# Performance work log

Measured on AMD Instinct MI355X. Metric: run time of the kernel, lower is better.

The kernel has to match this reference:

```python
import math
import jax, jax.numpy as jnp
import numpy as np

MAX_LEN = 1024

def _sinusoidal_pe(seq_len, d_model):
    pos = jnp.arange(seq_len, dtype=jnp.float32)[:, None]
    div = jnp.exp(jnp.arange(0, d_model, 2, dtype=jnp.float32) * (-math.log(10000.0) / d_model))
    ang = pos * div  # [S, D/2]
    pe = jnp.zeros((seq_len, d_model), dtype=jnp.float32)
    pe = pe.at[:, 0::2].set(jnp.sin(ang))
    pe = pe.at[:, 1::2].set(jnp.cos(ang))
    return pe

def setup_inputs() -> dict:
    key = jax.random.key(0)
    ks = jax.random.split(key, 4)
    B, S, D, H = 4, 1024, 1024, 16
    x = jax.random.normal(ks[0], (B, S, D), dtype=jnp.float32)
    gamma = jnp.ones((D,), dtype=jnp.float32)
    beta = jnp.zeros((D,), dtype=jnp.float32)
    w_pos = jax.random.normal(ks[1], (2 * D, D), dtype=jnp.float32) * (1.0 / math.sqrt(D))
    w_tok = jax.random.normal(ks[2], (3 * D, D), dtype=jnp.float32) * (1.0 / math.sqrt(D))
    bias_table = jax.random.normal(ks[3], (2 * MAX_LEN, H), dtype=jnp.float32) * 0.02
    return {"x": x, "gamma": gamma, "beta": beta, "w_pos": w_pos, "w_tok": w_tok, "bias_table": bias_table}

def reference(x, gamma, beta, w_pos, w_tok, bias_table):
    B, S, D = x.shape
    H = bias_table.shape[1]
    dh = D // H
    scale = 1.0 / math.sqrt(2 * dh)

    # untied positional scores (identical across batch)
    pe = _sinusoidal_pe(S, D)                      # [S, D]
    pos = pe @ w_pos.T                             # [S, 2D]
    pos_k, pos_q = pos[:, :D], pos[:, D:]
    pos_k = pos_k.reshape(S, H, dh)
    pos_q = pos_q.reshape(S, H, dh)
    pos_attn = jnp.einsum('qhd,khd->hqk', pos_q, pos_k)  # [H, S, S]

    # token scores
    mu = jnp.mean(x, axis=-1, keepdims=True)
    var = jnp.mean((x - mu) ** 2, axis=-1, keepdims=True)
    xn = (x - mu) / jnp.sqrt(var + 1e-5) * gamma + beta
    tok = xn @ w_tok.T                             # [B, S, 3D]
    tok_k, tok_q, tok_v = jnp.split(tok, 3, axis=-1)
    tok_k = tok_k.reshape(B, S, H, dh)
    tok_q = tok_q.reshape(B, S, H, dh)
    tok_v = tok_v.reshape(B, S, H, dh)
    tok_attn = jnp.einsum('bqhd,bkhd->bhqk', tok_q, tok_k)  # [B, H, S, S]

    attn = (tok_attn + pos_attn[None]) / scale

    # relative-position bias
    rel = jnp.arange(S)[None, :] - jnp.arange(S)[:, None] + MAX_LEN  # [S, S]
    bias = bias_table[rel]                         # [S, S, H]
    attn = attn + jnp.transpose(bias, (2, 0, 1))[None]

    attn = jax.nn.softmax(attn, axis=-1)
    out = jnp.einsum('bhqk,bkhd->bqhd', attn, tok_v)
    return out.reshape(B, S, D)
```

## Files before the change

kernel.cpp:

```cpp
#include <hip/hip_runtime.h>
#include <math.h>

#define SB 1024
#define DM 1024
#define BB 4
#define NH 16
#define DH 64
#define ML 1024

typedef __attribute__((ext_vector_type(8))) short short8;
typedef __attribute__((ext_vector_type(8))) _Float16 half8;
typedef __attribute__((ext_vector_type(4))) float f32x4;
typedef unsigned short u16;

#define S_BARRIER() __builtin_amdgcn_s_barrier()
#define SCHED_FENCE() __builtin_amdgcn_sched_barrier(0)
#define WAITV(N) asm volatile("s_waitcnt vmcnt(" #N ")" ::: "memory")
#define WAITLGKM() asm volatile("s_waitcnt lgkmcnt(0)" ::: "memory")
#define WAITVL() asm volatile("s_waitcnt vmcnt(0) lgkmcnt(0)" ::: "memory")

__device__ __forceinline__ u16 f2bf(float x) {
  unsigned u = __float_as_uint(x);
  u += 0x7fffu + ((u >> 16) & 1u);
  return (u16)(u >> 16);
}
__device__ __forceinline__ float bf2f(u16 h) { return __uint_as_float((unsigned)h << 16); }

__device__ __forceinline__ void async16(void* lds, const void* g) {
  __builtin_amdgcn_global_load_lds(
      (const __attribute__((address_space(1))) unsigned*)g,
      (__attribute__((address_space(3))) unsigned*)lds, 16, 0, 0);
}


__device__ __forceinline__ void pack16_body(int rt, int t, const float* __restrict__ src,
    _Float16* __restrict__ dH, _Float16* __restrict__ dL, float scale) {
  int r16 = t >> 4, ks = t & 15;
  const float* sp = src + (size_t)(rt * 16 + r16) * 1024 + ks * 64;
  float v[64];
  #pragma unroll
  for (int i = 0; i < 16; ++i) {
    float4 f = *(const float4*)(sp + i * 4);
    v[i*4+0] = f.x; v[i*4+1] = f.y; v[i*4+2] = f.z; v[i*4+3] = f.w;
  }
  #pragma unroll
  for (int hf = 0; hf < 2; ++hf) {
    int kt = ks * 2 + hf;
    #pragma unroll
    for (int gg = 0; gg < 4; ++gg) {
      half8 hv, lv;
      #pragma unroll
      for (int j = 0; j < 8; ++j) {
        float x = v[hf * 32 + gg * 8 + j] * scale;
        _Float16 h = (_Float16)x;
        hv[j] = h;
        lv[j] = (_Float16)(x - (float)h);
      }
      size_t off = ((size_t)(rt * 32 + kt) * 64 + r16 + gg * 16) * 8;
      *(half8*)(dH + off) = hv;
      *(half8*)(dL + off) = lv;
    }
  }
}

__device__ __forceinline__ void pe_pack_body(int rt, int t,
    _Float16* __restrict__ dH, _Float16* __restrict__ dL) {
  int r16 = t >> 4, ks = t & 15;
  int p = rt * 16 + r16;
  float v[64];
  #pragma unroll
  for (int i = 0; i < 32; ++i) {
    int c0 = ks * 64 + 2 * i;
    float div = expf((float)c0 * (-9.210340371976184f / (float)DM));
    float ang = (float)p * div;
    v[2*i]   = sinf(ang);
    v[2*i+1] = cosf(ang);
  }
  #pragma unroll
  for (int hf = 0; hf < 2; ++hf) {
    int kt = ks * 2 + hf;
    #pragma unroll
    for (int gg = 0; gg < 4; ++gg) {
      half8 hv, lv;
      #pragma unroll
      for (int j = 0; j < 8; ++j) {
        float x = v[hf * 32 + gg * 8 + j];
        _Float16 h = (_Float16)x;
        hv[j] = h;
        lv[j] = (_Float16)(x - (float)h);
      }
      size_t off = ((size_t)(rt * 32 + kt) * 64 + r16 + gg * 16) * 8;
      *(half8*)(dH + off) = hv;
      *(half8*)(dL + off) = lv;
    }
  }
}

__device__ __forceinline__ void ln_pack_body(int rt, int t, const float* __restrict__ x,
    const float* __restrict__ gamma, const float* __restrict__ beta,
    _Float16* __restrict__ dH, _Float16* __restrict__ dL) {
  int r16 = t >> 4, ks = t & 15;
  const float* sp = x + (size_t)(rt * 16 + r16) * 1024 + ks * 64;
  float v[64];
  float s1 = 0.f, s2 = 0.f;
  #pragma unroll
  for (int i = 0; i < 16; ++i) {
    float4 f = *(const float4*)(sp + i * 4);
    v[i*4+0] = f.x; v[i*4+1] = f.y; v[i*4+2] = f.z; v[i*4+3] = f.w;
    s1 += f.x + f.y + f.z + f.w;
    s2 += f.x*f.x + f.y*f.y + f.z*f.z + f.w*f.w;
  }
  #pragma unroll
  for (int off = 1; off < 16; off <<= 1) {
    s1 += __shfl_xor(s1, off, 64);
    s2 += __shfl_xor(s2, off, 64);
  }
  float mu = s1 * (1.0f / 1024.0f);
  float var = s2 * (1.0f / 1024.0f) - mu * mu;
  float rstd = rsqrtf(var + 1e-5f);
  #pragma unroll
  for (int hf = 0; hf < 2; ++hf) {
    int kt = ks * 2 + hf;
    #pragma unroll
    for (int gg = 0; gg < 4; ++gg) {
      const float* gp = gamma + ks * 64 + hf * 32 + gg * 8;
      const float* bp = beta  + ks * 64 + hf * 32 + gg * 8;
      half8 hv, lv;
      #pragma unroll
      for (int j = 0; j < 8; ++j) {
        float xn = (v[hf * 32 + gg * 8 + j] - mu) * rstd * gp[j] + bp[j];
        _Float16 h = (_Float16)xn;
        hv[j] = h;
        lv[j] = (_Float16)(xn - (float)h);
      }
      size_t off = ((size_t)(rt * 32 + kt) * 64 + r16 + gg * 16) * 8;
      *(half8*)(dH + off) = hv;
      *(half8*)(dL + off) = lv;
    }
  }
}

__global__ __launch_bounds__(256) void prep_all(
    const float* __restrict__ x, const float* __restrict__ gamma,
    const float* __restrict__ beta,
    const float* __restrict__ w_pos, const float* __restrict__ w_tok,
    _Float16* __restrict__ peH, _Float16* __restrict__ peL,
    _Float16* __restrict__ xnH, _Float16* __restrict__ xnL,
    _Float16* __restrict__ wpH, _Float16* __restrict__ wpL,
    _Float16* __restrict__ wtH, _Float16* __restrict__ wtL) {
  int bid = blockIdx.x;
  int t = threadIdx.x;
  if (bid < 64)       pe_pack_body(bid, t, peH, peL);
  else if (bid < 320) ln_pack_body(bid - 64, t, x, gamma, beta, xnH, xnL);
  else if (bid < 448) pack16_body(bid - 320, t, w_pos, wpH, wpL, 32.0f);
  else                pack16_body(bid - 448, t, w_tok, wtH, wtL, 32.0f);
}


__device__ __forceinline__ void stage_gemm(bool split, int wv, int lane,
    _Float16* Lb, const _Float16* AH, const _Float16* AL, const _Float16* BH,
    int mt0, int nt0, int kt) {
  if (split) {
    #pragma unroll
    for (int rd = 0; rd < 8; ++rd) {
      int ci = rd * 4 + wv;
      const _Float16* src;
      if (ci < 16) {
        int mt = ci >> 1, pl = ci & 1;
        src = (pl ? AL : AH) + ((size_t)((mt0 + mt) * 32 + kt) * 64 + lane) * 8;
      } else {
        src = BH + ((size_t)((nt0 + ci - 16) * 32 + kt) * 64 + lane) * 8;
      }
      async16(&Lb[ci * 512], src);
    }
  } else {
    #pragma unroll
    for (int rd = 0; rd < 6; ++rd) {
      int idx = wv * 6 + rd;
      int ci = (idx < 8) ? (idx * 2) : (idx + 8);
      const _Float16* src;
      if (ci < 16) {
        src = AH + ((size_t)((mt0 + (ci >> 1)) * 32 + kt) * 64 + lane) * 8;
      } else {
        src = BH + ((size_t)((nt0 + ci - 16) * 32 + kt) * 64 + lane) * 8;
      }
      async16(&Lb[ci * 512], src);
    }
  }
}

__global__ __launch_bounds__(256, 2) void gemm16p(
    const _Float16* __restrict__ AtH, const _Float16* __restrict__ AtL,
    const _Float16* __restrict__ ApH, const _Float16* __restrict__ ApL,
    const _Float16* __restrict__ BtH, const _Float16* __restrict__ BtL,
    const _Float16* __restrict__ BpH, const _Float16* __restrict__ BpL,
    u16* __restrict__ KtfH, u16* __restrict__ KtfL,
    u16* __restrict__ KpfH, u16* __restrict__ KpfL,
    u16* __restrict__ QH, u16* __restrict__ QL,
    u16* __restrict__ pQH, u16* __restrict__ pQL,
    u16* __restrict__ vF, float sK, float sQ, float sV) {
  __shared__ _Float16 L[2][32 * 512];
  int t = threadIdx.x;
  int wv = t >> 6, lane = t & 63;
  int wm = wv >> 1, wn = wv & 1;
  int r16 = lane & 15, g = lane >> 4;

  int phys = blockIdx.x;
  int bid = (phys & 7) * 56 + (phys >> 3);
  bool isPos = (bid >= 384);
  int idx = isPos ? bid - 384 : bid;
  int n0, m0;
  const _Float16 *AH, *AL, *BH, *BL;
  if (isPos) { n0 = (idx & 7) * 256;  m0 = (idx >> 3) * 128;
               AH = ApH; AL = ApL; BH = BpH; BL = BpL; }
  else       { n0 = (idx % 12) * 256; m0 = (idx / 12) * 128;
               AH = AtH; AL = AtL; BH = BtH; BL = BtL; }
  int mt0 = m0 >> 4, nt0 = n0 >> 4;
  bool split = isPos || (n0 < 2048);

  f32x4 acc[4][8];
  #pragma unroll
  for (int i = 0; i < 4; ++i)
    #pragma unroll
    for (int j = 0; j < 8; ++j) acc[i][j] = (f32x4){0.f, 0.f, 0.f, 0.f};

  stage_gemm(split, wv, lane, &L[0][0], AH, AL, BH, mt0, nt0, 0);

  for (int kt = 0; kt < 32; ++kt) {
    _Float16* Lc = &L[kt & 1][0];
    half8 blo[8];
    if (split) {
      #pragma unroll
      for (int j = 0; j < 8; ++j) {
        int ntg = nt0 + wn * 8 + j;
        blo[j] = *(const half8*)(BL + ((size_t)(ntg * 32 + kt) * 64 + lane) * 8);
      }
    }
    SCHED_FENCE();
    if (kt < 31)
      stage_gemm(split, wv, lane, &L[(kt + 1) & 1][0], AH, AL, BH, mt0, nt0, kt + 1);
    if (split) { if (kt < 31) WAITV(16); else WAITV(8); }
    else       { if (kt < 31) WAITV(6);  else WAITV(0); }
    S_BARRIER();
    SCHED_FENCE();

    half8 ah[4], al[4];
    #pragma unroll
    for (int i = 0; i < 4; ++i)
      ah[i] = *(const half8*)&Lc[(((wm * 4 + i) * 2 + 0) * 512) + lane * 8];
    if (split) {
      #pragma unroll
      for (int i = 0; i < 4; ++i)
        al[i] = *(const half8*)&Lc[(((wm * 4 + i) * 2 + 1) * 512) + lane * 8];
    }
    #pragma unroll
    for (int j = 0; j < 8; ++j) {
      half8 bh = *(const half8*)&Lc[((16 + wn * 8 + j) * 512) + lane * 8];
      #pragma unroll
      for (int i = 0; i < 4; ++i) {
        acc[i][j] = __builtin_amdgcn_mfma_f32_16x16x32_f16(ah[i], bh, acc[i][j], 0, 0, 0);
        if (split) {
          acc[i][j] = __builtin_amdgcn_mfma_f32_16x16x32_f16(al[i], bh, acc[i][j], 0, 0, 0);
          acc[i][j] = __builtin_amdgcn_mfma_f32_16x16x32_f16(ah[i], blo[j], acc[i][j], 0, 0, 0);
        }
      }
    }
    WAITLGKM();
    S_BARRIER();
    SCHED_FENCE();
  }

  int band = n0 >> 10;
  u16* fKH = isPos ? KpfH : KtfH;
  u16* fKL = isPos ? KpfL : KtfL;
  u16* qHo = isPos ? pQH  : QH;
  u16* qLo = isPos ? pQL  : QL;
  if (band == 1) {
    #pragma unroll
    for (int i = 0; i < 4; ++i)
      #pragma unroll
      for (int j = 0; j < 8; ++j) {
        int lc = (n0 & 1023) + wn * 128 + j * 16 + r16;
        #pragma unroll
        for (int reg = 0; reg < 4; ++reg) {
          int row = m0 + wm * 64 + i * 16 + g * 4 + reg;
          float cv = acc[i][j][reg] * sQ;
          u16 hi = f2bf(cv);
          qHo[(size_t)row * 1024 + lc] = hi;
          qLo[(size_t)row * 1024 + lc] = f2bf(cv - bf2f(hi));
        }
      }
  } else if (band == 0) {
    #pragma unroll
    for (int i = 0; i < 4; ++i)
      #pragma unroll
      for (int j = 0; j < 8; ++j) {
        int colg = n0 + wn * 128 + j * 16 + r16;
        int h = colg >> 6, dc = colg & 63;
        #pragma unroll
        for (int reg = 0; reg < 4; ++reg) {
          int row = m0 + wm * 64 + i * 16 + g * 4 + reg;
          int bhK = (row >> 10) * NH + h;
          size_t a = ((size_t)((bhK * 64 + ((row & 1023) >> 4)) * 2 + (dc >> 5)) << 9)
                   + ((row & 15) + 16 * ((dc >> 3) & 3)) * 8 + (dc & 7);
          float cv = acc[i][j][reg] * sK;
          u16 hi = f2bf(cv);
          fKH[a] = hi;
          fKL[a] = f2bf(cv - bf2f(hi));
        }
      }
  } else {
    #pragma unroll
    for (int i = 0; i < 4; ++i)
      #pragma unroll
      for (int j = 0; j < 8; ++j) {
        int colg = (n0 & 1023) + wn * 128 + j * 16 + r16;
        int h = colg >> 6, dc = colg & 63;
        #pragma unroll
        for (int reg = 0; reg < 4; ++reg) {
          int row = m0 + wm * 64 + i * 16 + g * 4 + reg;
          int s = row & 1023;
          size_t a = ((size_t)((((row >> 10) * NH + h) * 32 + (s >> 5)) * 4 + (dc >> 4)) << 9)
                   + ((s >> 3) & 3) * 128 + (s & 7) + (dc & 15) * 8;
          vF[a] = f2bf(acc[i][j][reg] * sV);
        }
      }
  }
}

__global__ __launch_bounds__(256, 2) void gemm16m(
    const _Float16* __restrict__ AtH, const _Float16* __restrict__ AtL,
    const _Float16* __restrict__ ApH, const _Float16* __restrict__ ApL,
    const float* __restrict__ Wt, const float* __restrict__ Wp,
    u16* __restrict__ KtfH, u16* __restrict__ KtfL,
    u16* __restrict__ KpfH, u16* __restrict__ KpfL,
    u16* __restrict__ QH, u16* __restrict__ QL,
    u16* __restrict__ pQH, u16* __restrict__ pQL,
    u16* __restrict__ vF, float sK, float sQ, float sV) {
  __shared__ _Float16 L[48 * 512];
  int t = threadIdx.x;
  int wv = t >> 6, lane = t & 63;
  int wm = wv >> 1, wn = wv & 1;
  int r16 = lane & 15, g = lane >> 4;

  int phys = blockIdx.x;
  int bid = (phys & 7) * 56 + (phys >> 3);
  bool isPos = (bid >= 384);
  int idx = isPos ? bid - 384 : bid;
  int n0, m0;
  const _Float16 *AH, *AL;
  const float* W;
  if (isPos) { n0 = (idx & 7) * 256;  m0 = (idx >> 3) * 128; AH = ApH; AL = ApL; W = Wp; }
  else       { n0 = (idx % 12) * 256; m0 = (idx / 12) * 128; AH = AtH; AL = AtL; W = Wt; }
  int mt0 = m0 >> 4, nt0 = n0 >> 4;
  bool split = isPos || (n0 < 2048);

  f32x4 acc[4][8];
  #pragma unroll
  for (int i = 0; i < 4; ++i)
    #pragma unroll
    for (int j = 0; j < 8; ++j) acc[i][j] = (f32x4){0.f, 0.f, 0.f, 0.f};

  for (int kt = 0; kt < 32; ++kt) {
    __syncthreads();
    #pragma unroll
    for (int rd = 0; rd < 4; ++rd) {
      int ci = rd * 4 + wv;
      int mt = ci >> 1, pl = ci & 1;
      if (!split && pl) continue;
      const _Float16* src = (pl ? AL : AH)
          + ((size_t)((mt0 + mt) * 32 + kt) * 64 + lane) * 8;
      async16(&L[ci * 512], src);
    }
    #pragma unroll
    for (int tt = 0; tt < 4; ++tt) {
      int nt = wv * 4 + tt;
      const float* wsrc = W + (size_t)((nt0 + nt) * 16 + r16) * 1024 + kt * 32 + g * 8;
      float4 w0 = *(const float4*)wsrc;
      float4 w1 = *(const float4*)(wsrc + 4);
      float wvv[8] = {w0.x, w0.y, w0.z, w0.w, w1.x, w1.y, w1.z, w1.w};
      half8 hv, lv;
      #pragma unroll
      for (int j = 0; j < 8; ++j) {
        float xx = wvv[j] * 32.0f;
        _Float16 h = (_Float16)xx;
        hv[j] = h;
        lv[j] = (_Float16)(xx - (float)h);
      }
      *(half8*)&L[(16 + nt) * 512 + lane * 8] = hv;
      if (split) *(half8*)&L[(32 + nt) * 512 + lane * 8] = lv;
    }
    __syncthreads();

    half8 ah[4], al[4];
    #pragma unroll
    for (int i = 0; i < 4; ++i)
      ah[i] = *(const half8*)&L[(((wm * 4 + i) * 2 + 0) * 512) + lane * 8];
    if (split) {
      #pragma unroll
      for (int i = 0; i < 4; ++i)
        al[i] = *(const half8*)&L[(((wm * 4 + i) * 2 + 1) * 512) + lane * 8];
    }
    #pragma unroll
    for (int j = 0; j < 8; ++j) {
      half8 bh = *(const half8*)&L[((16 + wn * 8 + j) * 512) + lane * 8];
      #pragma unroll
      for (int i = 0; i < 4; ++i) {
        acc[i][j] = __builtin_amdgcn_mfma_f32_16x16x32_f16(ah[i], bh, acc[i][j], 0, 0, 0);
        if (split) {
          half8 bl = *(const half8*)&L[((32 + wn * 8 + j) * 512) + lane * 8];
          acc[i][j] = __builtin_amdgcn_mfma_f32_16x16x32_f16(al[i], bh, acc[i][j], 0, 0, 0);
          acc[i][j] = __builtin_amdgcn_mfma_f32_16x16x32_f16(ah[i], bl, acc[i][j], 0, 0, 0);
        }
      }
    }
  }

  int band = n0 >> 10;
  u16* fKH = isPos ? KpfH : KtfH;
  u16* fKL = isPos ? KpfL : KtfL;
  u16* qHo = isPos ? pQH  : QH;
  u16* qLo = isPos ? pQL  : QL;
  if (band == 1) {
    #pragma unroll
    for (int i = 0; i < 4; ++i)
      #pragma unroll
      for (int j = 0; j < 8; ++j) {
        int lc = (n0 & 1023) + wn * 128 + j * 16 + r16;
        #pragma unroll
        for (int reg = 0; reg < 4; ++reg) {
          int row = m0 + wm * 64 + i * 16 + g * 4 + reg;
          float cv = acc[i][j][reg] * sQ;
          u16 hi = f2bf(cv);
          qHo[(size_t)row * 1024 + lc] = hi;
          qLo[(size_t)row * 1024 + lc] = f2bf(cv - bf2f(hi));
        }
      }
  } else if (band == 0) {
    #pragma unroll
    for (int i = 0; i < 4; ++i)
      #pragma unroll
      for (int j = 0; j < 8; ++j) {
        int colg = n0 + wn * 128 + j * 16 + r16;
        int h = colg >> 6, dc = colg & 63;
        #pragma unroll
        for (int reg = 0; reg < 4; ++reg) {
          int row = m0 + wm * 64 + i * 16 + g * 4 + reg;
          int bhK = (row >> 10) * NH + h;
          size_t a = ((size_t)((bhK * 64 + ((row & 1023) >> 4)) * 2 + (dc >> 5)) << 9)
                   + ((row & 15) + 16 * ((dc >> 3) & 3)) * 8 + (dc & 7);
          float cv = acc[i][j][reg] * sK;
          u16 hi = f2bf(cv);
          fKH[a] = hi;
          fKL[a] = f2bf(cv - bf2f(hi));
        }
      }
  } else {
    #pragma unroll
    for (int i = 0; i < 4; ++i)
      #pragma unroll
      for (int j = 0; j < 8; ++j) {
        int colg = (n0 & 1023) + wn * 128 + j * 16 + r16;
        int h = colg >> 6, dc = colg & 63;
        #pragma unroll
        for (int reg = 0; reg < 4; ++reg) {
          int row = m0 + wm * 64 + i * 16 + g * 4 + reg;
          int s = row & 1023;
          size_t a = ((size_t)((((row >> 10) * NH + h) * 32 + (s >> 5)) * 4 + (dc >> 4)) << 9)
                   + ((s >> 3) & 3) * 128 + (s & 7) + (dc & 15) * 8;
          vF[a] = f2bf(acc[i][j][reg] * sV);
        }
      }
  }
}

__device__ __forceinline__ void stage_attn(u16* Klds,
    const u16* ktH, const u16* ktL, const u16* kpH, const u16* kpL,
    const u16* vb, int wv, int lo) {
  int p0 = wv * 512, p1 = (wv + 4) * 512;
  async16(&Klds[0 * 4096 + p0], ktH + p0 + lo);
  async16(&Klds[0 * 4096 + p1], ktH + p1 + lo);
  async16(&Klds[1 * 4096 + p0], ktL + p0 + lo);
  async16(&Klds[1 * 4096 + p1], ktL + p1 + lo);
  async16(&Klds[2 * 4096 + p0], kpH + p0 + lo);
  async16(&Klds[2 * 4096 + p1], kpH + p1 + lo);
  async16(&Klds[3 * 4096 + p0], kpL + p0 + lo);
  async16(&Klds[3 * 4096 + p1], kpL + p1 + lo);
  async16(&Klds[4 * 4096 + p0], vb + p0 + lo);
  async16(&Klds[4 * 4096 + p1], vb + p1 + lo);
}

__global__ __launch_bounds__(256, 2) void attn_mfma11(
    const u16* __restrict__ KtfH, const u16* __restrict__ KtfL,
    const u16* __restrict__ KpfH, const u16* __restrict__ KpfL,
    const u16* __restrict__ QHg, const u16* __restrict__ QLg,
    const u16* __restrict__ pQH, const u16* __restrict__ pQL,
    const u16* __restrict__ Vf,
    const float* __restrict__ bt,
    float* __restrict__ out) {
  __shared__ u16 Klds[5 * 4096];
  __shared__ float biasL[2 * ML];
  __shared__ u16 Pb[4][16 * 72];

  int phys = blockIdx.x;
  int bid = (phys & 7) * 64 + (phys >> 3);
  int qt = bid & 7;
  int bh = bid >> 3;
  int b = bh >> 4, h = bh & 15;
  int q0 = qt * 128;
  int t = threadIdx.x;
  int wv = t >> 6, lane = t & 63;
  int g = lane >> 4, r16 = lane & 15;
  int lo = lane * 8;

  #pragma unroll
  for (int k = 0; k < 8; ++k)
    biasL[t + k * 256] = bt[(size_t)(t + k * 256) * NH + h];

  short8 qhi[2][4], qlo[2][4];
  #pragma unroll
  for (int cc = 0; cc < 2; ++cc) {
    int qrow = q0 + wv * 32 + cc * 16 + r16;
    #pragma unroll
    for (int c = 0; c < 4; ++c) {
      if (c < 2) {
        size_t off = (size_t)(b * SB + qrow) * 1024 + h * DH + c * 32 + g * 8;
        qhi[cc][c] = *(const short8*)(QHg + off);
        qlo[cc][c] = *(const short8*)(QLg + off);
      } else {
        size_t off = (size_t)qrow * 1024 + h * DH + (c - 2) * 32 + g * 8;
        qhi[cc][c] = *(const short8*)(pQH + off);
        qlo[cc][c] = *(const short8*)(pQL + off);
      }
    }
  }

  f32x4 O[2][4];
  #pragma unroll
  for (int cc = 0; cc < 2; ++cc)
    #pragma unroll
    for (int dt = 0; dt < 4; ++dt) O[cc][dt] = (f32x4){0.f, 0.f, 0.f, 0.f};
  float m_run[2][4], l_run[2][4];
  #pragma unroll
  for (int cc = 0; cc < 2; ++cc)
    #pragma unroll
    for (int reg = 0; reg < 4; ++reg) { m_run[cc][reg] = -3e38f; l_run[cc][reg] = 0.f; }

  int qb0 = q0 + wv * 32 + g * 4;
  const u16* ktHb = KtfH + (size_t)(bh * 64) * 1024;
  const u16* ktLb = KtfL + (size_t)(bh * 64) * 1024;
  const u16* kpHb = KpfH + (size_t)(h * 64) * 1024;
  const u16* kpLb = KpfL + (size_t)(h * 64) * 1024;
  const u16* vb   = Vf   + (size_t)(bh * 32) * 2048;
  int bb = ML + r16 - qb0;

  stage_attn(Klds, ktHb, ktLb, kpHb, kpLb, vb, wv, lo);

  for (int ktr = 0; ktr < 16; ++ktr) {
    WAITVL();
    S_BARRIER();
    SCHED_FENCE();

    float bias[2][4][4];
    #pragma unroll
    for (int nt = 0; nt < 4; ++nt)
      #pragma unroll
      for (int reg = 0; reg < 4; ++reg) {
        bias[0][nt][reg] = biasL[bb + nt * 16 - reg];
        bias[1][nt][reg] = biasL[bb - 16 + nt * 16 - reg];
      }

    f32x4 S[2][4];
    #pragma unroll
    for (int nt = 0; nt < 4; ++nt) {
      f32x4 a0 = (f32x4){0.f, 0.f, 0.f, 0.f};
      f32x4 a1 = (f32x4){0.f, 0.f, 0.f, 0.f};
      #pragma unroll
      for (int c = 0; c < 4; ++c) {
        int ch = (c < 2) ? 0 : 2;
        int co = c & 1;
        short8 bhi = *(const short8*)&Klds[(ch + 0) * 4096 + nt * 1024 + co * 512 + lo];
        short8 blo = *(const short8*)&Klds[(ch + 1) * 4096 + nt * 1024 + co * 512 + lo];
        a0 = __builtin_amdgcn_mfma_f32_16x16x32_bf16(qhi[0][c], bhi, a0, 0, 0, 0);
        a1 = __builtin_amdgcn_mfma_f32_16x16x32_bf16(qhi[1][c], bhi, a1, 0, 0, 0);
        a0 = __builtin_amdgcn_mfma_f32_16x16x32_bf16(qlo[0][c], bhi, a0, 0, 0, 0);
        a1 = __builtin_amdgcn_mfma_f32_16x16x32_bf16(qlo[1][c], bhi, a1, 0, 0, 0);
        a0 = __builtin_amdgcn_mfma_f32_16x16x32_bf16(qhi[0][c], blo, a0, 0, 0, 0);
        a1 = __builtin_amdgcn_mfma_f32_16x16x32_bf16(qhi[1][c], blo, a1, 0, 0, 0);
      }
      S[0][nt] = a0; S[1][nt] = a1;
    }

    short8 vfrag[2][4];
    #pragma unroll
    for (int kc = 0; kc < 2; ++kc)
      #pragma unroll
      for (int dt = 0; dt < 4; ++dt)
        vfrag[kc][dt] = *(const short8*)&Klds[4 * 4096 + (kc * 4 + dt) * 512 + lo];

    WAITLGKM();
    S_BARRIER();
    SCHED_FENCE();
    if (ktr < 15) {
      ktHb += 4096; ktLb += 4096; kpHb += 4096; kpLb += 4096; vb += 4096;
      stage_attn(Klds, ktHb, ktLb, kpHb, kpLb, vb, wv, lo);
    }
    SCHED_FENCE();

    #pragma unroll
    for (int cc = 0; cc < 2; ++cc)
      #pragma unroll
      for (int nt = 0; nt < 4; ++nt)
        #pragma unroll
        for (int reg = 0; reg < 4; ++reg)
          S[cc][nt][reg] += bias[cc][nt][reg];

    float tm[2][4], al[2][4];
    #pragma unroll
    for (int cc = 0; cc < 2; ++cc)
      #pragma unroll
      for (int reg = 0; reg < 4; ++reg)
        tm[cc][reg] = fmaxf(fmaxf(S[cc][0][reg], S[cc][1][reg]),
                            fmaxf(S[cc][2][reg], S[cc][3][reg]));
    #pragma unroll
    for (int off = 1; off < 16; off <<= 1)
      #pragma unroll
      for (int cc = 0; cc < 2; ++cc)
        #pragma unroll
        for (int reg = 0; reg < 4; ++reg)
          tm[cc][reg] = fmaxf(tm[cc][reg], __shfl_xor(tm[cc][reg], off, 64));
    #pragma unroll
    for (int cc = 0; cc < 2; ++cc)
      #pragma unroll
      for (int reg = 0; reg < 4; ++reg) {
        float mn = fmaxf(m_run[cc][reg], tm[cc][reg]);
        al[cc][reg] = __expf(m_run[cc][reg] - mn);
        m_run[cc][reg] = mn;
      }
    float ts[2][4] = {{0.f, 0.f, 0.f, 0.f}, {0.f, 0.f, 0.f, 0.f}};
    #pragma unroll
    for (int cc = 0; cc < 2; ++cc)
      #pragma unroll
      for (int nt = 0; nt < 4; ++nt)
        #pragma unroll
        for (int reg = 0; reg < 4; ++reg) {
          float p = __expf(S[cc][nt][reg] - m_run[cc][reg]);
          S[cc][nt][reg] = p;
          ts[cc][reg] += p;
        }
    #pragma unroll
    for (int cc = 0; cc < 2; ++cc)
      #pragma unroll
      for (int reg = 0; reg < 4; ++reg)
        l_run[cc][reg] = l_run[cc][reg] * al[cc][reg] + ts[cc][reg];
    #pragma unroll
    for (int cc = 0; cc < 2; ++cc)
      #pragma unroll
      for (int dt = 0; dt < 4; ++dt)
        #pragma unroll
        for (int reg = 0; reg < 4; ++reg)
          O[cc][dt][reg] *= al[cc][reg];

    #pragma unroll
    for (int cc = 0; cc < 2; ++cc) {
      u16* pb = Pb[wv];
      #pragma unroll
      for (int nt = 0; nt < 4; ++nt)
        #pragma unroll
        for (int reg = 0; reg < 4; ++reg)
          pb[(g * 4 + reg) * 72 + nt * 16 + r16] = f2bf(S[cc][nt][reg]);
      #pragma unroll
      for (int kc = 0; kc < 2; ++kc) {
        short8 pa = *(const short8*)&Pb[wv][r16 * 72 + kc * 32 + g * 8];
        #pragma unroll
        for (int dt = 0; dt < 4; ++dt)
          O[cc][dt] = __builtin_amdgcn_mfma_f32_16x16x32_bf16(pa, vfrag[kc][dt], O[cc][dt], 0, 0, 0);
      }
    }

    bb += 64;
  }

  #pragma unroll
  for (int off = 1; off < 16; off <<= 1)
    #pragma unroll
    for (int cc = 0; cc < 2; ++cc)
      #pragma unroll
      for (int reg = 0; reg < 4; ++reg)
        l_run[cc][reg] += __shfl_xor(l_run[cc][reg], off, 64);
  #pragma unroll
  for (int cc = 0; cc < 2; ++cc)
    #pragma unroll
    for (int reg = 0; reg < 4; ++reg) l_run[cc][reg] = 1.0f / l_run[cc][reg];
  #pragma unroll
  for (int cc = 0; cc < 2; ++cc)
    #pragma unroll
    for (int dt = 0; dt < 4; ++dt)
      #pragma unroll
      for (int reg = 0; reg < 4; ++reg)
        out[(size_t)(b * SB + qb0 + cc * 16 + reg) * DM + h * DH + dt * 16 + r16] =
            O[cc][dt][reg] * l_run[cc][reg];
}

extern "C" void kernel_launch(void* const* d_in, const int* in_sizes, int n_in,
                              void* d_out, int out_size, void* d_ws, size_t ws_size,
                              hipStream_t stream) {
  const float* x     = (const float*)d_in[0];
  const float* gamma = (const float*)d_in[1];
  const float* beta  = (const float*)d_in[2];
  const float* w_pos = (const float*)d_in[3];
  const float* w_tok = (const float*)d_in[4];
  const float* bt    = (const float*)d_in[5];
  float* out = (float*)d_out;
  float* ws  = (float*)d_ws;
  const size_t M1 = 1u << 20;
  const float IS = 11.313708498984761f;

  u16 *KtfH, *KtfL, *KpfH, *KpfL, *QH, *QL, *posQH, *posQL, *Vf;

  if (ws_size >= 22 * M1 * 4) {
    _Float16* peH = (_Float16*)(ws);
    _Float16* peL = (_Float16*)(ws + M1 / 2);
    _Float16* xnH = (_Float16*)(ws + 1 * M1);
    _Float16* xnL = (_Float16*)(ws + 3 * M1);
    _Float16* wpH = (_Float16*)(ws + 5 * M1);
    _Float16* wpL = (_Float16*)(ws + 6 * M1);
    _Float16* wtH = (_Float16*)(ws + 7 * M1);
    _Float16* wtL = (_Float16*)(ws + 8 * M1 + M1/2);
    KpfH  = (u16*)(ws + 10 * M1);
    KpfL  = (u16*)(ws + 10 * M1 + M1 / 2);
    posQH = (u16*)(ws + 11 * M1);
    posQL = (u16*)(ws + 11 * M1 + M1 / 2);
    KtfH  = (u16*)(ws + 12 * M1);
    KtfL  = (u16*)(ws + 14 * M1);
    QH    = (u16*)(ws + 16 * M1);
    QL    = (u16*)(ws + 18 * M1);
    Vf    = (u16*)(ws + 20 * M1);

    prep_all<<<640, 256, 0, stream>>>(x, gamma, beta, w_pos, w_tok,
        peH, peL, xnH, xnL, wpH, wpL, wtH, wtL);
    gemm16p<<<448, 256, 0, stream>>>(
        xnH, xnL, peH, peL, wtH, wtL, wpH, wpL,
        KtfH, KtfL, KpfH, KpfL, QH, QL, posQH, posQL, Vf,
        1.0f / 32.0f, IS / 32.0f, 1.0f / 32.0f);
  } else {
    _Float16* peH = (_Float16*)(ws);
    _Float16* peL = (_Float16*)(ws + M1 / 2);
    _Float16* xnH = (_Float16*)(ws + 1 * M1);
    _Float16* xnL = (_Float16*)(ws + 3 * M1);
    KpfH  = (u16*)(ws + 5 * M1);
    KpfL  = (u16*)(ws + 5 * M1 + M1 / 2);
    posQH = (u16*)(ws + 6 * M1);
    posQL = (u16*)(ws + 6 * M1 + M1 / 2);
    KtfH  = (u16*)(ws + 7 * M1);
    KtfL  = (u16*)(ws + 9 * M1);
    QH    = (u16*)(ws + 11 * M1);
    QL    = (u16*)(ws + 13 * M1);
    Vf    = (u16*)(ws + 15 * M1);

    prep_all<<<320, 256, 0, stream>>>(x, gamma, beta, w_pos, w_tok,
        peH, peL, xnH, xnL, (_Float16*)nullptr, (_Float16*)nullptr,
        (_Float16*)nullptr, (_Float16*)nullptr);
    gemm16m<<<448, 256, 0, stream>>>(
        xnH, xnL, peH, peL, w_tok, w_pos,
        KtfH, KtfL, KpfH, KpfL, QH, QL, posQH, posQL, Vf,
        1.0f / 32.0f, IS / 32.0f, 1.0f / 32.0f);
  }

  attn_mfma11<<<BB * NH * (SB / 128), 256, 0, stream>>>(
      KtfH, KtfL, KpfH, KpfL, QH, QL, posQH, posQL, Vf, bt, out);
}
```

Baseline: 256.4 us.

## Stage B low plane through LDS single-buffer and use fast sin/cos in PE pack

The projection GEMM now stages the B low-precision plane into shared memory alongside the A and B high planes, instead of loading it straight from global memory into registers. In exchange it drops the double-buffered async prefetch in favour of a single 48-tile buffer guarded by __syncthreads on every k-step. This removes the overlap between loading the next tile and computing the current one, and adds more LDS traffic per step. Separately, the positional-encoding pack switches to exp2f and the fast __sinf/__cosf intrinsics, which may lose accuracy at large angles.

```diff
diff --git a/kernel.cpp b/kernel.cpp
--- a/kernel.cpp
+++ b/kernel.cpp
@@ -71,10 +71,10 @@
   #pragma unroll
   for (int i = 0; i < 32; ++i) {
     int c0 = ks * 64 + 2 * i;
-    float div = expf((float)c0 * (-9.210340371976184f / (float)DM));
+    float div = exp2f((float)c0 * (-0.01297628162065376f));
     float ang = (float)p * div;
-    v[2*i]   = sinf(ang);
-    v[2*i+1] = cosf(ang);
+    v[2*i]   = __sinf(ang);
+    v[2*i+1] = __cosf(ang);
   }
   #pragma unroll
   for (int hf = 0; hf < 2; ++hf) {
@@ -157,19 +157,21 @@
 }
 
 
-__device__ __forceinline__ void stage_gemm(bool split, int wv, int lane,
-    _Float16* Lb, const _Float16* AH, const _Float16* AL, const _Float16* BH,
-    int mt0, int nt0, int kt) {
+__device__ __forceinline__ void stage48(bool split, int wv, int lane,
+    _Float16* Lb, const _Float16* AH, const _Float16* AL,
+    const _Float16* BH, const _Float16* BL, int mt0, int nt0, int kt) {
   if (split) {
     #pragma unroll
-    for (int rd = 0; rd < 8; ++rd) {
+    for (int rd = 0; rd < 12; ++rd) {
       int ci = rd * 4 + wv;
       const _Float16* src;
       if (ci < 16) {
-        int mt = ci >> 1, pl = ci & 1;
-        src = (pl ? AL : AH) + ((size_t)((mt0 + mt) * 32 + kt) * 64 + lane) * 8;
+        src = ((ci & 1) ? AL : AH)
+            + ((size_t)((mt0 + (ci >> 1)) * 32 + kt) * 64 + lane) * 8;
+      } else if (ci < 32) {
+        src = BH + ((size_t)((nt0 + ci - 16) * 32 + kt) * 64 + lane) * 8;
       } else {
-        src = BH + ((size_t)((nt0 + ci - 16) * 32 + kt) * 64 + lane) * 8;
+        src = BL + ((size_t)((nt0 + ci - 32) * 32 + kt) * 64 + lane) * 8;
       }
       async16(&Lb[ci * 512], src);
     }
@@ -179,11 +181,8 @@
       int idx = wv * 6 + rd;
       int ci = (idx < 8) ? (idx * 2) : (idx + 8);
       const _Float16* src;
-      if (ci < 16) {
-        src = AH + ((size_t)((mt0 + (ci >> 1)) * 32 + kt) * 64 + lane) * 8;
-      } else {
-        src = BH + ((size_t)((nt0 + ci - 16) * 32 + kt) * 64 + lane) * 8;
-      }
+      if (ci < 16) src = AH + ((size_t)((mt0 + (ci >> 1)) * 32 + kt) * 64 + lane) * 8;
+      else         src = BH + ((size_t)((nt0 + ci - 16) * 32 + kt) * 64 + lane) * 8;
       async16(&Lb[ci * 512], src);
     }
   }
@@ -199,7 +198,7 @@
     u16* __restrict__ QH, u16* __restrict__ QL,
     u16* __restrict__ pQH, u16* __restrict__ pQL,
     u16* __restrict__ vF, float sK, float sQ, float sV) {
-  __shared__ _Float16 L[2][32 * 512];
+  __shared__ _Float16 L[48 * 512];
   int t = threadIdx.x;
   int wv = t >> 6, lane = t & 63;
   int wm = wv >> 1, wn = wv & 1;
@@ -224,50 +223,33 @@
     #pragma unroll
     for (int j = 0; j < 8; ++j) acc[i][j] = (f32x4){0.f, 0.f, 0.f, 0.f};
 
-  stage_gemm(split, wv, lane, &L[0][0], AH, AL, BH, mt0, nt0, 0);
-
   for (int kt = 0; kt < 32; ++kt) {
-    _Float16* Lc = &L[kt & 1][0];
-    half8 blo[8];
+    __syncthreads();
+    stage48(split, wv, lane, &L[0], AH, AL, BH, BL, mt0, nt0, kt);
+    __syncthreads();
+
+    half8 ah[4], al[4];
+    #pragma unroll
+    for (int i = 0; i < 4; ++i)
+      ah[i] = *(const half8*)&L[(((wm * 4 + i) * 2 + 0) * 512) + lane * 8];
     if (split) {
       #pragma unroll
-      for (int j = 0; j < 8; ++j) {
-        int ntg = nt0 + wn * 8 + j;
-        blo[j] = *(const half8*)(BL + ((size_t)(ntg * 32 + kt) * 64 + lane) * 8);
-      }
-    }
-    SCHED_FENCE();
-    if (kt < 31)
-      stage_gemm(split, wv, lane, &L[(kt + 1) & 1][0], AH, AL, BH, mt0, nt0, kt + 1);
-    if (split) { if (kt < 31) WAITV(16); else WAITV(8); }
-    else       { if (kt < 31) WAITV(6);  else WAITV(0); }
-    S_BARRIER();
-    SCHED_FENCE();
-
-    half8 ah[4], al[4];
-    #pragma unroll
-    for (int i = 0; i < 4; ++i)
-      ah[i] = *(const half8*)&Lc[(((wm * 4 + i) * 2 + 0) * 512) + lane * 8];
-    if (split) {
-      #pragma unroll
       for (int i = 0; i < 4; ++i)
-        al[i] = *(const half8*)&Lc[(((wm * 4 + i) * 2 + 1) * 512) + lane * 8];
+        al[i] = *(const half8*)&L[(((wm * 4 + i) * 2 + 1) * 512) + lane * 8];
     }
     #pragma unroll
     for (int j = 0; j < 8; ++j) {
-      half8 bh = *(const half8*)&Lc[((16 + wn * 8 + j) * 512) + lane * 8];
+      half8 bh = *(const half8*)&L[((16 + wn * 8 + j) * 512) + lane * 8];
       #pragma unroll
       for (int i = 0; i < 4; ++i) {
         acc[i][j] = __builtin_amdgcn_mfma_f32_16x16x32_f16(ah[i], bh, acc[i][j], 0, 0, 0);
         if (split) {
+          half8 bl = *(const half8*)&L[((32 + wn * 8 + j) * 512) + lane * 8];
           acc[i][j] = __builtin_amdgcn_mfma_f32_16x16x32_f16(al[i], bh, acc[i][j], 0, 0, 0);
-          acc[i][j] = __builtin_amdgcn_mfma_f32_16x16x32_f16(ah[i], blo[j], acc[i][j], 0, 0, 0);
-        }
-      }
-    }
-    WAITLGKM();
-    S_BARRIER();
-    SCHED_FENCE();
+          acc[i][j] = __builtin_amdgcn_mfma_f32_16x16x32_f16(ah[i], bl, acc[i][j], 0, 0, 0);
+        }
+      }
+    }
   }
 
   int band = n0 >> 10;
```

Result: slower. 265.2 us (+3.4%).
